# Kernel tuning notes

Hardware: AMD Instinct MI355X
Metric: run time of the kernel (lower is better)

Reference implementation:

```python
import jax, jax.numpy as jnp
import numpy as np

ALPHA = 0.2  # LeakyReLU negative slope


def setup_inputs() -> dict:
    key = jax.random.key(0)
    ks = jax.random.split(key, 6)
    B, N, F_IN, F_OUT = 4, 4096, 128, 128
    return {
        "input": jax.random.normal(ks[0], (B, N, F_IN), dtype=jnp.float32),
        "adj": jax.random.uniform(ks[1], (B, N, N), dtype=jnp.float32),
        "W": jax.random.normal(ks[2], (F_IN, F_OUT), dtype=jnp.float32) * (np.sqrt(2.0) / np.sqrt(F_IN)),
        "a1": jax.random.normal(ks[3], (F_OUT, 1), dtype=jnp.float32) * 0.1,
        "a2": jax.random.normal(ks[4], (F_OUT, 1), dtype=jnp.float32) * 0.1,
        "bias": jax.random.normal(ks[5], (N, F_OUT), dtype=jnp.float32) * 0.02,
    }


def reference(input, adj, W, a1, a2, bias):
    # h = X @ W : [B, N, F_out]
    h = jnp.einsum("bnf,fo->bno", input, W)
    # additive attention scores: e[b,i,j] = leakyrelu(f1[b,i] + f2[b,j])
    f1 = h @ a1            # [B, N, 1]
    f2 = h @ a2            # [B, N, 1]
    e = f1 + jnp.swapaxes(f2, 1, 2)        # [B, N, N]
    e = jnp.where(e >= 0, e, ALPHA * e)    # LeakyReLU
    # NOTE: original multiplies adj into scores (not -inf masking) and
    # softmaxes over dim=1 (the first node axis), faithfully reproduced.
    attention = jax.nn.softmax(adj * e, axis=1)  # [B, N, N]
    # dropout p=0 / eval mode -> identity
    h_prime = jnp.einsum("bij,bjo->bio", attention, h) + bias[None, :, :]
    # in_features == out_features -> plain residual
    return h_prime + input
```

## Files before the change

kernel.cpp:

```cpp
#include <hip/hip_runtime.h>
#include <hip/hip_bf16.h>

typedef short short8 __attribute__((ext_vector_type(8)));
typedef float f32x4 __attribute__((ext_vector_type(4)));
typedef unsigned short u16;
typedef u16 u16x8 __attribute__((ext_vector_type(8)));

static constexpr float kAlpha = 0.2f;

static __device__ inline u16 f2bf(float f) {
  __hip_bfloat16 h = __float2bfloat16(f);
  return *reinterpret_cast<u16*>(&h);
}
static __device__ inline float bf2f(u16 v) {
  unsigned int u = ((unsigned int)v) << 16;
  return __uint_as_float(u);
}

__global__ __launch_bounds__(256) void k1_hW(const float* __restrict__ X,
                                             const float* __restrict__ W,
                                             u16* __restrict__ hbT) {
  int row0 = blockIdx.x * 8;
  int o = threadIdx.x & 127;
  int g = threadIdx.x >> 7;
  __shared__ float Xs[8][128];
#pragma unroll
  for (int s = 0; s < 4; ++s) {
    int idx = threadIdx.x + s * 256;
    Xs[idx >> 7][idx & 127] = X[(size_t)row0 * 128 + idx];
  }
  __syncthreads();
  float acc[4] = {0.f, 0.f, 0.f, 0.f};
  for (int k = 0; k < 128; ++k) {
    float w = W[k * 128 + o];
#pragma unroll
    for (int s = 0; s < 4; ++s) acc[s] += Xs[g + 2 * s][k] * w;
  }
  int b = row0 >> 12;
  int n0 = row0 & 4095;
#pragma unroll
  for (int s = 0; s < 4; ++s)
    hbT[((size_t)b * 128 + o) * 4096 + n0 + g + 2 * s] = f2bf(acc[s]);
}

__global__ __launch_bounds__(256) void k1b_f(const u16* __restrict__ hbT,
                                             const float* __restrict__ a1,
                                             const float* __restrict__ a2,
                                             float* __restrict__ f1,
                                             float* __restrict__ f2) {
  int idx = blockIdx.x * 256 + threadIdx.x;
  int b = idx >> 12;
  int n = idx & 4095;
  const u16* base = hbT + (size_t)b * 128 * 4096 + n;
  float s1 = 0.f, s2 = 0.f;
  for (int o = 0; o < 128; ++o) {
    float h = bf2f(base[(size_t)o * 4096]);
    s1 += h * a1[o];
    s2 += h * a2[o];
  }
  f1[idx] = s1;
  f2[idx] = s2;
}

__global__ __launch_bounds__(256) void k2_dpart(const float* __restrict__ adj,
                                                const float* __restrict__ f1,
                                                const float* __restrict__ f2,
                                                float* __restrict__ dpart) {
  int bid = blockIdx.x;
  int ic = bid & 31;
  int jt = (bid >> 5) & 15;
  int b = bid >> 9;
  int t = threadIdx.x;
  int c = t & 63, r = t >> 6;
  int j = jt * 256 + c * 4;
  const size_t badj = (size_t)b * 4096 * 4096;
  f32x4 f2v = *reinterpret_cast<const f32x4*>(&f2[b * 4096 + j]);
  const float* f1p = f1 + b * 4096;
  int row0 = ic * 128 + r;
  f32x4 sum = (f32x4){0.f, 0.f, 0.f, 0.f};
#pragma unroll 8
  for (int s = 0; s < 32; ++s) {
    int row = row0 + 4 * s;
    f32x4 a = *reinterpret_cast<const f32x4*>(&adj[badj + (size_t)row * 4096 + j]);
    float f1r = f1p[row];
#pragma unroll
    for (int k = 0; k < 4; ++k) {
      float e = f1r + f2v[k];
      e = e >= 0.f ? e : kAlpha * e;
      sum[k] += __expf(a[k] * e);
    }
  }
  __shared__ f32x4 red[256];
  red[t] = sum;
  __syncthreads();
  if (t < 64) {
    f32x4 tt = red[t] + red[t + 64] + red[t + 128] + red[t + 192];
    *reinterpret_cast<f32x4*>(&dpart[(size_t)(b * 32 + ic) * 4096 + j]) = tt;
  }
}

__global__ __launch_bounds__(256) void k2b_scale(const float* __restrict__ dpart,
                                                 const u16* __restrict__ hbT,
                                                 u16* __restrict__ hs) {
  int idx = blockIdx.x * 256 + threadIdx.x;
  int b = idx >> 12, j = idx & 4095;
  float s = 0.f;
#pragma unroll
  for (int ic = 0; ic < 32; ++ic) s += dpart[(size_t)(b * 32 + ic) * 4096 + j];
  float rd = 1.0f / s;
  const u16* src = hbT + (size_t)b * 128 * 4096 + j;
  u16* dst = hs + (size_t)b * 128 * 4096 + j;
#pragma unroll 4
  for (int o = 0; o < 128; ++o) {
    dst[(size_t)o * 4096] = f2bf(bf2f(src[(size_t)o * 4096]) * rd);
  }
}

#define LROW 72
#define BARRIER()                                     \
  {                                                   \
    asm volatile("s_waitcnt lgkmcnt(0)" ::: "memory"); \
    __builtin_amdgcn_s_barrier();                     \
  }
__global__ __launch_bounds__(512) void k3_out(
    const float* __restrict__ adj, const u16* __restrict__ hs,
    const float* __restrict__ f1, const float* __restrict__ f2,
    const float* __restrict__ bias, const float* __restrict__ input,
    float* __restrict__ out) {
  int bid = blockIdx.x;
  int b = bid >> 6;
  int i0 = (bid & 63) * 64;
  int t = threadIdx.x;
  int lane = t & 63;
  int w = t >> 6;

  __shared__ u16 As[2][64 * LROW];
  __shared__ u16 Bs[2][128 * LROW];
  __shared__ float f2s[4096];

  const size_t badj = (size_t)b * 4096 * 4096;
  const u16* hb = hs + (size_t)b * 128 * 4096;

  {
    const f32x4* src = reinterpret_cast<const f32x4*>(f2 + b * 4096);
    f32x4* dst = reinterpret_cast<f32x4*>(f2s);
    dst[t] = src[t];
    dst[t + 512] = src[t + 512];
  }
  __syncthreads();

  int rr = t >> 3;
  int c0 = (t & 7) * 8;
  int bo = t >> 2;
  int bc0 = (t & 3) * 16;

  float f1v = f1[b * 4096 + i0 + rr];

  f32x4 acc[4];
#pragma unroll
  for (int n = 0; n < 4; ++n) acc[n] = (f32x4){0.f, 0.f, 0.f, 0.f};

  int rg = w & 3;
  int ch = w >> 2;

  f32x4 raA0, raA1, raB0, raB1, raC0, raC1, raD0, raD1;
  u16x8 rbA0, rbA1, rbB0, rbB1, rbC0, rbC1, rbD0, rbD1;

#define PREFETCH(S, J0)                                                              \
  {                                                                                  \
    int jj = (J0) & 4095;          \
    const f32x4* ap = reinterpret_cast<const f32x4*>(                                \
        adj + badj + (size_t)(i0 + rr) * 4096 + jj + c0);                            \
    ra##S##0 = ap[0];                                                                \
    ra##S##1 = ap[1];                                                                \
    const u16x8* bp =                                                                \
        reinterpret_cast<const u16x8*>(hb + (size_t)bo * 4096 + jj + bc0);           \
    rb##S##0 = bp[0];                                                                \
    rb##S##1 = bp[1];                                                                \
  }

#define STORE(S, J0, BUF)                                                            \
  {                                                                                  \
    f32x4 e0 = *reinterpret_cast<const f32x4*>(&f2s[(J0) + c0]);                     \
    f32x4 e1 = *reinterpret_cast<const f32x4*>(&f2s[(J0) + c0 + 4]);                 \
    u16x8 pv;                                                                        \
    _Pragma("unroll") for (int k = 0; k < 4; ++k) {                                  \
      float e = f1v + e0[k];                                                         \
      e = e >= 0.f ? e : kAlpha * e;                                                 \
      pv[k] = f2bf(__expf(ra##S##0[k] * e));                                         \
    }                                                                                \
    _Pragma("unroll") for (int k = 0; k < 4; ++k) {                                  \
      float e = f1v + e1[k];                                                         \
      e = e >= 0.f ? e : kAlpha * e;                                                 \
      pv[k + 4] = f2bf(__expf(ra##S##1[k] * e));                                     \
    }                                                                                \
    *reinterpret_cast<u16x8*>(&As[BUF][rr * LROW + c0]) = pv;                        \
    *reinterpret_cast<u16x8*>(&Bs[BUF][bo * LROW + bc0]) = rb##S##0;                 \
    *reinterpret_cast<u16x8*>(&Bs[BUF][bo * LROW + bc0 + 8]) = rb##S##1;             \
  }

#define DOMFMA(BUF)                                                                  \
  {                                                                                  \
    _Pragma("unroll") for (int kk = 0; kk < 64; kk += 32) {                          \
      short8 af = *reinterpret_cast<const short8*>(                                  \
          &As[BUF][(16 * rg + (lane & 15)) * LROW + kk + (lane >> 4) * 8]);          \
      _Pragma("unroll") for (int n = 0; n < 4; ++n) {                                \
        short8 bf = *reinterpret_cast<const short8*>(                                \
            &Bs[BUF][(64 * ch + n * 16 + (lane & 15)) * LROW + kk +                  \
                     (lane >> 4) * 8]);                                              \
        acc[n] = __builtin_amdgcn_mfma_f32_16x16x32_bf16(af, bf, acc[n], 0, 0, 0);   \
      }                                                                              \
    }                                                                                \
  }

  PREFETCH(A, 0);
  PREFETCH(B, 64);
  PREFETCH(C, 128);
  PREFETCH(D, 192);

  for (int j0 = 0; j0 < 4096; j0 += 256) {
    STORE(A, j0, 0);
    BARRIER();
    DOMFMA(0);
    PREFETCH(A, j0 + 256);
    STORE(B, j0 + 64, 1);
    BARRIER();
    DOMFMA(1);
    PREFETCH(B, j0 + 320);
    STORE(C, j0 + 128, 0);
    BARRIER();
    DOMFMA(0);
    PREFETCH(C, j0 + 384);
    STORE(D, j0 + 192, 1);
    BARRIER();
    DOMFMA(1);
    PREFETCH(D, j0 + 448);
  }

  int colbase = ch * 64 + (lane & 15);
  int rowbase = i0 + rg * 16 + (lane >> 4) * 4;
#pragma unroll
  for (int n = 0; n < 4; ++n) {
    int o = colbase + n * 16;
#pragma unroll
    for (int q = 0; q < 4; ++q) {
      int i = rowbase + q;
      size_t oidx = ((size_t)b * 4096 + i) * 128 + o;
      out[oidx] = acc[n][q] + bias[i * 128 + o] + input[oidx];
    }
  }
}

extern "C" void kernel_launch(void* const* d_in, const int* in_sizes, int n_in,
                              void* d_out, int out_size, void* d_ws, size_t ws_size,
                              hipStream_t stream) {
  const float* input = (const float*)d_in[0];
  const float* adj = (const float*)d_in[1];
  const float* W = (const float*)d_in[2];
  const float* a1 = (const float*)d_in[3];
  const float* a2 = (const float*)d_in[4];
  const float* bias = (const float*)d_in[5];
  float* out = (float*)d_out;

  char* ws = (char*)d_ws;
  u16* hbT = (u16*)(ws);
  float* f1 = (float*)(ws + 4194304);
  float* f2 = (float*)(ws + 4259840);
  float* dpart = (float*)(ws + 4325376);
  u16* hs = (u16*)(ws + 6422528);

  k1_hW<<<2048, 256, 0, stream>>>(input, W, hbT);
  k1b_f<<<64, 256, 0, stream>>>(hbT, a1, a2, f1, f2);
  k2_dpart<<<2048, 256, 0, stream>>>(adj, f1, f2, dpart);
  k2b_scale<<<64, 256, 0, stream>>>(dpart, hbT, hs);
  k3_out<<<256, 512, 0, stream>>>(adj, hs, f1, f2, bias, input, out);
}
```

Measured before the change: 141.5 us.

## Materialize bf16 attention weights once per batch instead of re-reading adj in GEMM

The first pass now writes the exponentiated scores as a bf16 matrix while also computing the softmax column sums. The GEMM kernel then reads that bf16 matrix directly as its A operand. This removes the second full fp32 read of adj and the recomputation of exp. The work runs per batch so each 32MB score buffer can stay resident in the large last-level cache between producer and consumer. The GEMM also gains a 4-way split over K, with a separate reduction kernel that adds bias and the residual. In exchange it issues four times as many launches, puts fewer blocks in each one (the scale kernel gets only 16), and writes and re-reads the partial sums.

```diff
diff --git a/kernel.cpp b/kernel.cpp
--- a/kernel.cpp
+++ b/kernel.cpp
@@ -4,6 +4,7 @@
 typedef short short8 __attribute__((ext_vector_type(8)));
 typedef float f32x4 __attribute__((ext_vector_type(4)));
 typedef unsigned short u16;
+typedef u16 u16x4 __attribute__((ext_vector_type(4)));
 typedef u16 u16x8 __attribute__((ext_vector_type(8)));
 
 static constexpr float kAlpha = 0.2f;
@@ -62,100 +63,81 @@
   f2[idx] = s2;
 }
 
-__global__ __launch_bounds__(256) void k2_dpart(const float* __restrict__ adj,
-                                                const float* __restrict__ f1,
-                                                const float* __restrict__ f2,
-                                                float* __restrict__ dpart) {
+__global__ __launch_bounds__(256) void k2p(const float* __restrict__ adjb,
+                                           const float* __restrict__ f1b,
+                                           const float* __restrict__ f2b,
+                                           u16* __restrict__ ptil,
+                                           float* __restrict__ dpart) {
   int bid = blockIdx.x;
   int ic = bid & 31;
-  int jt = (bid >> 5) & 15;
-  int b = bid >> 9;
+  int jt = bid >> 5;
   int t = threadIdx.x;
   int c = t & 63, r = t >> 6;
   int j = jt * 256 + c * 4;
-  const size_t badj = (size_t)b * 4096 * 4096;
-  f32x4 f2v = *reinterpret_cast<const f32x4*>(&f2[b * 4096 + j]);
-  const float* f1p = f1 + b * 4096;
+  f32x4 f2v = *reinterpret_cast<const f32x4*>(&f2b[j]);
   int row0 = ic * 128 + r;
   f32x4 sum = (f32x4){0.f, 0.f, 0.f, 0.f};
-#pragma unroll 8
+#pragma unroll 4
   for (int s = 0; s < 32; ++s) {
     int row = row0 + 4 * s;
-    f32x4 a = *reinterpret_cast<const f32x4*>(&adj[badj + (size_t)row * 4096 + j]);
-    float f1r = f1p[row];
+    f32x4 a = *reinterpret_cast<const f32x4*>(&adjb[(size_t)row * 4096 + j]);
+    float f1r = f1b[row];
+    u16x4 pv;
 #pragma unroll
     for (int k = 0; k < 4; ++k) {
       float e = f1r + f2v[k];
       e = e >= 0.f ? e : kAlpha * e;
-      sum[k] += __expf(a[k] * e);
+      float p = __expf(a[k] * e);
+      sum[k] += p;
+      pv[k] = f2bf(p);
     }
+    *reinterpret_cast<u16x4*>(&ptil[(size_t)row * 4096 + j]) = pv;
   }
   __shared__ f32x4 red[256];
   red[t] = sum;
   __syncthreads();
   if (t < 64) {
     f32x4 tt = red[t] + red[t + 64] + red[t + 128] + red[t + 192];
-    *reinterpret_cast<f32x4*>(&dpart[(size_t)(b * 32 + ic) * 4096 + j]) = tt;
-  }
-}
-
-__global__ __launch_bounds__(256) void k2b_scale(const float* __restrict__ dpart,
-                                                 const u16* __restrict__ hbT,
-                                                 u16* __restrict__ hs) {
-  int idx = blockIdx.x * 256 + threadIdx.x;
-  int b = idx >> 12, j = idx & 4095;
+    *reinterpret_cast<f32x4*>(&dpart[(size_t)ic * 4096 + j]) = tt;
+  }
+}
+
+__global__ __launch_bounds__(256) void k2bs(const float* __restrict__ dpart,
+                                            const u16* __restrict__ hbTb,
+                                            u16* __restrict__ hs) {
+  int j = blockIdx.x * 256 + threadIdx.x;
   float s = 0.f;
 #pragma unroll
-  for (int ic = 0; ic < 32; ++ic) s += dpart[(size_t)(b * 32 + ic) * 4096 + j];
+  for (int ic = 0; ic < 32; ++ic) s += dpart[(size_t)ic * 4096 + j];
   float rd = 1.0f / s;
-  const u16* src = hbT + (size_t)b * 128 * 4096 + j;
-  u16* dst = hs + (size_t)b * 128 * 4096 + j;
 #pragma unroll 4
   for (int o = 0; o < 128; ++o) {
-    dst[(size_t)o * 4096] = f2bf(bf2f(src[(size_t)o * 4096]) * rd);
+    hs[(size_t)o * 4096 + j] = f2bf(bf2f(hbTb[(size_t)o * 4096 + j]) * rd);
   }
 }
 
 #define LROW 72
-#define BARRIER()                                     \
-  {                                                   \
+#define BARRIER()                                      \
+  {                                                    \
     asm volatile("s_waitcnt lgkmcnt(0)" ::: "memory"); \
-    __builtin_amdgcn_s_barrier();                     \
-  }
-__global__ __launch_bounds__(512) void k3_out(
-    const float* __restrict__ adj, const u16* __restrict__ hs,
-    const float* __restrict__ f1, const float* __restrict__ f2,
-    const float* __restrict__ bias, const float* __restrict__ input,
-    float* __restrict__ out) {
+    __builtin_amdgcn_s_barrier();                      \
+  }
+__global__ __launch_bounds__(512) void k3p(const u16* __restrict__ ptil,
+                                           const u16* __restrict__ hs,
+                                           float* __restrict__ parts) {
   int bid = blockIdx.x;
-  int b = bid >> 6;
   int i0 = (bid & 63) * 64;
+  int q = bid >> 6;
+  int jbase = q * 1024;
   int t = threadIdx.x;
   int lane = t & 63;
   int w = t >> 6;
 
-  __shared__ u16 As[2][64 * LROW];
   __shared__ u16 Bs[2][128 * LROW];
-  __shared__ float f2s[4096];
-
-  const size_t badj = (size_t)b * 4096 * 4096;
-  const u16* hb = hs + (size_t)b * 128 * 4096;
-
-  {
-    const f32x4* src = reinterpret_cast<const f32x4*>(f2 + b * 4096);
-    f32x4* dst = reinterpret_cast<f32x4*>(f2s);
-    dst[t] = src[t];
-    dst[t + 512] = src[t + 512];
-  }
-  __syncthreads();
-
-  int rr = t >> 3;
-  int c0 = (t & 7) * 8;
+
   int bo = t >> 2;
   int bc0 = (t & 3) * 16;
 
-  float f1v = f1[b * 4096 + i0 + rr];
-
   f32x4 acc[4];
 #pragma unroll
   for (int n = 0; n < 4; ++n) acc[n] = (f32x4){0.f, 0.f, 0.f, 0.f};
@@ -163,92 +145,94 @@
   int rg = w & 3;
   int ch = w >> 2;
 
-  f32x4 raA0, raA1, raB0, raB1, raC0, raC1, raD0, raD1;
+  const u16* arow = ptil + (size_t)(i0 + 16 * rg + (lane & 15)) * 4096 + (lane >> 4) * 8;
+
+  u16x8 afA0, afA1, afB0, afB1, afC0, afC1, afD0, afD1;
   u16x8 rbA0, rbA1, rbB0, rbB1, rbC0, rbC1, rbD0, rbD1;
 
-#define PREFETCH(S, J0)                                                              \
+#define PREFETCH(S, J0)                                                     \
+  {                                                                         \
+    int jj = (J0) & 4095;          \
+    af##S##0 = *reinterpret_cast<const u16x8*>(arow + jj);                  \
+    af##S##1 = *reinterpret_cast<const u16x8*>(arow + jj + 32);             \
+    const u16x8* bp =                                                       \
+        reinterpret_cast<const u16x8*>(hs + (size_t)bo * 4096 + jj + bc0);  \
+    rb##S##0 = bp[0];                                                       \
+    rb##S##1 = bp[1];                                                       \
+  }
+
+#define STORE(S, BUF)                                                       \
+  {                                                                         \
+    *reinterpret_cast<u16x8*>(&Bs[BUF][bo * LROW + bc0]) = rb##S##0;        \
+    *reinterpret_cast<u16x8*>(&Bs[BUF][bo * LROW + bc0 + 8]) = rb##S##1;    \
+  }
+
+#define DOMFMA(BUF, S)                                                               \
   {                                                                                  \
-    int jj = (J0) & 4095;          \
-    const f32x4* ap = reinterpret_cast<const f32x4*>(                                \
-        adj + badj + (size_t)(i0 + rr) * 4096 + jj + c0);                            \
-    ra##S##0 = ap[0];                                                                \
-    ra##S##1 = ap[1];                                                                \
-    const u16x8* bp =                                                                \
-        reinterpret_cast<const u16x8*>(hb + (size_t)bo * 4096 + jj + bc0);           \
-    rb##S##0 = bp[0];                                                                \
-    rb##S##1 = bp[1];                                                                \
-  }
-
-#define STORE(S, J0, BUF)                                                            \
-  {                                                                                  \
-    f32x4 e0 = *reinterpret_cast<const f32x4*>(&f2s[(J0) + c0]);                     \
-    f32x4 e1 = *reinterpret_cast<const f32x4*>(&f2s[(J0) + c0 + 4]);                 \
-    u16x8 pv;                                                                        \
-    _Pragma("unroll") for (int k = 0; k < 4; ++k) {                                  \
-      float e = f1v + e0[k];                                                         \
-      e = e >= 0.f ? e : kAlpha * e;                                                 \
-      pv[k] = f2bf(__expf(ra##S##0[k] * e));                                         \
+    _Pragma("unroll") for (int n = 0; n < 4; ++n) {                                  \
+      short8 bf = *reinterpret_cast<const short8*>(                                  \
+          &Bs[BUF][(64 * ch + n * 16 + (lane & 15)) * LROW + (lane >> 4) * 8]);      \
+      acc[n] = __builtin_amdgcn_mfma_f32_16x16x32_bf16(                              \
+          *reinterpret_cast<const short8*>(&af##S##0), bf, acc[n], 0, 0, 0);         \
     }                                                                                \
-    _Pragma("unroll") for (int k = 0; k < 4; ++k) {                                  \
-      float e = f1v + e1[k];                                                         \
-      e = e >= 0.f ? e : kAlpha * e;                                                 \
-      pv[k + 4] = f2bf(__expf(ra##S##1[k] * e));                                     \
+    _Pragma("unroll") for (int n = 0; n < 4; ++n) {                                  \
+      short8 bf = *reinterpret_cast<const short8*>(                                  \
+          &Bs[BUF][(64 * ch + n * 16 + (lane & 15)) * LROW + 32 + (lane >> 4) * 8]); \
+      acc[n] = __builtin_amdgcn_mfma_f32_16x16x32_bf16(                              \
+          *reinterpret_cast<const short8*>(&af##S##1), bf, acc[n], 0, 0, 0);         \
     }                                                                                \
-    *reinterpret_cast<u16x8*>(&As[BUF][rr * LROW + c0]) = pv;                        \
-    *reinterpret_cast<u16x8*>(&Bs[BUF][bo * LROW + bc0]) = rb##S##0;                 \
-    *reinterpret_cast<u16x8*>(&Bs[BUF][bo * LROW + bc0 + 8]) = rb##S##1;             \
-  }
-
-#define DOMFMA(BUF)                                                                  \
-  {                                                                                  \
-    _Pragma("unroll") for (int kk = 0; kk < 64; kk += 32) {                          \
-      short8 af = *reinterpret_cast<const short8*>(                                  \
-          &As[BUF][(16 * rg + (lane & 15)) * LROW + kk + (lane >> 4) * 8]);          \
-      _Pragma("unroll") for (int n = 0; n < 4; ++n) {                                \
-        short8 bf = *reinterpret_cast<const short8*>(                                \
-            &Bs[BUF][(64 * ch + n * 16 + (lane & 15)) * LROW + kk +                  \
-                     (lane >> 4) * 8]);                                              \
-        acc[n] = __builtin_amdgcn_mfma_f32_16x16x32_bf16(af, bf, acc[n], 0, 0, 0);   \
-      }                                                                              \
-    }                                                                                \
-  }
-
-  PREFETCH(A, 0);
-  PREFETCH(B, 64);
-  PREFETCH(C, 128);
-  PREFETCH(D, 192);
-
-  for (int j0 = 0; j0 < 4096; j0 += 256) {
-    STORE(A, j0, 0);
-    BARRIER();
-    DOMFMA(0);
+  }
+
+  PREFETCH(A, jbase);
+  PREFETCH(B, jbase + 64);
+  PREFETCH(C, jbase + 128);
+  PREFETCH(D, jbase + 192);
+
+  for (int j0 = jbase; j0 < jbase + 1024; j0 += 256) {
+    STORE(A, 0);
+    BARRIER();
+    DOMFMA(0, A);
     PREFETCH(A, j0 + 256);
-    STORE(B, j0 + 64, 1);
-    BARRIER();
-    DOMFMA(1);
+    STORE(B, 1);
+    BARRIER();
+    DOMFMA(1, B);
     PREFETCH(B, j0 + 320);
-    STORE(C, j0 + 128, 0);
-    BARRIER();
-    DOMFMA(0);
+    STORE(C, 0);
+    BARRIER();
+    DOMFMA(0, C);
     PREFETCH(C, j0 + 384);
-    STORE(D, j0 + 192, 1);
-    BARRIER();
-    DOMFMA(1);
+    STORE(D, 1);
+    BARRIER();
+    DOMFMA(1, D);
     PREFETCH(D, j0 + 448);
   }
 
   int colbase = ch * 64 + (lane & 15);
   int rowbase = i0 + rg * 16 + (lane >> 4) * 4;
+  float* pq = parts + (size_t)q * 4096 * 128;
 #pragma unroll
   for (int n = 0; n < 4; ++n) {
     int o = colbase + n * 16;
 #pragma unroll
-    for (int q = 0; q < 4; ++q) {
-      int i = rowbase + q;
-      size_t oidx = ((size_t)b * 4096 + i) * 128 + o;
-      out[oidx] = acc[n][q] + bias[i * 128 + o] + input[oidx];
+    for (int qq = 0; qq < 4; ++qq) {
+      pq[(size_t)(rowbase + qq) * 128 + o] = acc[n][qq];
     }
   }
+}
+
+__global__ __launch_bounds__(256) void k4r(const float* __restrict__ parts,
+                                           const float* __restrict__ bias,
+                                           const float* __restrict__ inputb,
+                                           float* __restrict__ outb) {
+  size_t v = (size_t)blockIdx.x * 256 + threadIdx.x;
+  size_t e = v * 4;
+  f32x4 s = *reinterpret_cast<const f32x4*>(&parts[e]);
+  s += *reinterpret_cast<const f32x4*>(&parts[e + 524288]);
+  s += *reinterpret_cast<const f32x4*>(&parts[e + 2 * 524288]);
+  s += *reinterpret_cast<const f32x4*>(&parts[e + 3 * 524288]);
+  s += *reinterpret_cast<const f32x4*>(&bias[e]);
+  s += *reinterpret_cast<const f32x4*>(&inputb[e]);
+  *reinterpret_cast<f32x4*>(&outb[e]) = s;
 }
 
 extern "C" void kernel_launch(void* const* d_in, const int* in_sizes, int n_in,
@@ -267,11 +251,24 @@
   float* f1 = (float*)(ws + 4194304);
   float* f2 = (float*)(ws + 4259840);
   float* dpart = (float*)(ws + 4325376);
-  u16* hs = (u16*)(ws + 6422528);
+  u16* hs = (u16*)(ws + 4849664);
+  u16* ptil = (u16*)(ws + 5898240);
+  float* parts = (float*)(ws + 39452672);
 
   k1_hW<<<2048, 256, 0, stream>>>(input, W, hbT);
   k1b_f<<<64, 256, 0, stream>>>(hbT, a1, a2, f1, f2);
-  k2_dpart<<<2048, 256, 0, stream>>>(adj, f1, f2, dpart);
-  k2b_scale<<<64, 256, 0, stream>>>(dpart, hbT, hs);
-  k3_out<<<256, 512, 0, stream>>>(adj, hs, f1, f2, bias, input, out);
-}
+
+  for (int b = 0; b < 4; ++b) {
+    const float* adjb = adj + (size_t)b * 4096 * 4096;
+    const float* f1b = f1 + b * 4096;
+    const float* f2b = f2 + b * 4096;
+    const u16* hbTb = hbT + (size_t)b * 128 * 4096;
+    const float* inputb = input + (size_t)b * 4096 * 128;
+    float* outb = out + (size_t)b * 4096 * 128;
+
+    k2p<<<512, 256, 0, stream>>>(adjb, f1b, f2b, ptil, dpart);
+    k2bs<<<16, 256, 0, stream>>>(dpart, hbTb, hs);
+    k3p<<<256, 512, 0, stream>>>(ptil, hs, parts);
+    k4r<<<512, 256, 0, stream>>>(parts, bias, inputb, outb);
+  }
+}
```

After: 207.9 us. +46.9%, slower.

## Halve k3 row tile to double grid, split k2b across output groups

Applied to the files above, without the earlier changes.

k3_out now handles 32 rows per block instead of 64, which doubles the grid to 512 blocks. Block IDs are remapped to spread batches across XCDs, and the f2 shared-memory staging is dropped in favour of per-tile register loads. Each wave computes a 16x32 output instead of 16x64. k2b_scale is split into 512 blocks, each covering 16 output features, so the small scaling kernel fills more CUs. The smaller tile reloads the hs B-tile for twice as many blocks, so L2 traffic on the h matrix rises.

```diff
diff --git a/kernel.cpp b/kernel.cpp
--- a/kernel.cpp
+++ b/kernel.cpp
@@ -4,6 +4,7 @@
 typedef short short8 __attribute__((ext_vector_type(8)));
 typedef float f32x4 __attribute__((ext_vector_type(4)));
 typedef unsigned short u16;
+typedef u16 u16x4 __attribute__((ext_vector_type(4)));
 typedef u16 u16x8 __attribute__((ext_vector_type(8)));
 
 static constexpr float kAlpha = 0.2f;
@@ -102,8 +103,11 @@
 __global__ __launch_bounds__(256) void k2b_scale(const float* __restrict__ dpart,
                                                  const u16* __restrict__ hbT,
                                                  u16* __restrict__ hs) {
-  int idx = blockIdx.x * 256 + threadIdx.x;
-  int b = idx >> 12, j = idx & 4095;
+  int bid = blockIdx.x;
+  int og = bid & 7;
+  int jb = (bid >> 3) & 15;
+  int b = bid >> 7;
+  int j = jb * 256 + threadIdx.x;
   float s = 0.f;
 #pragma unroll
   for (int ic = 0; ic < 32; ++ic) s += dpart[(size_t)(b * 32 + ic) * 4096 + j];
@@ -111,106 +115,93 @@
   const u16* src = hbT + (size_t)b * 128 * 4096 + j;
   u16* dst = hs + (size_t)b * 128 * 4096 + j;
 #pragma unroll 4
-  for (int o = 0; o < 128; ++o) {
+  for (int o = og * 16; o < og * 16 + 16; ++o) {
     dst[(size_t)o * 4096] = f2bf(bf2f(src[(size_t)o * 4096]) * rd);
   }
 }
 
 #define LROW 72
-#define BARRIER()                                     \
-  {                                                   \
+#define BARRIER()                                      \
+  {                                                    \
     asm volatile("s_waitcnt lgkmcnt(0)" ::: "memory"); \
-    __builtin_amdgcn_s_barrier();                     \
-  }
-__global__ __launch_bounds__(512) void k3_out(
+    __builtin_amdgcn_s_barrier();                      \
+  }
+__global__ __launch_bounds__(512, 4) void k3_out(
     const float* __restrict__ adj, const u16* __restrict__ hs,
     const float* __restrict__ f1, const float* __restrict__ f2,
     const float* __restrict__ bias, const float* __restrict__ input,
     float* __restrict__ out) {
-  int bid = blockIdx.x;
-  int b = bid >> 6;
-  int i0 = (bid & 63) * 64;
+  int bid0 = blockIdx.x;
+  int bid = ((bid0 & 7) << 6) | (bid0 >> 3);
+  int b = bid >> 7;
+  int i0 = (bid & 127) * 32;
   int t = threadIdx.x;
   int lane = t & 63;
   int w = t >> 6;
 
-  __shared__ u16 As[2][64 * LROW];
+  __shared__ u16 As[2][32 * LROW];
   __shared__ u16 Bs[2][128 * LROW];
-  __shared__ float f2s[4096];
 
   const size_t badj = (size_t)b * 4096 * 4096;
   const u16* hb = hs + (size_t)b * 128 * 4096;
-
-  {
-    const f32x4* src = reinterpret_cast<const f32x4*>(f2 + b * 4096);
-    f32x4* dst = reinterpret_cast<f32x4*>(f2s);
-    dst[t] = src[t];
-    dst[t + 512] = src[t + 512];
-  }
-  __syncthreads();
-
-  int rr = t >> 3;
-  int c0 = (t & 7) * 8;
+  const float* f2b = f2 + b * 4096;
+
+  int rr = t >> 4;
+  int c0 = (t & 15) * 4;
   int bo = t >> 2;
   int bc0 = (t & 3) * 16;
 
   float f1v = f1[b * 4096 + i0 + rr];
 
-  f32x4 acc[4];
-#pragma unroll
-  for (int n = 0; n < 4; ++n) acc[n] = (f32x4){0.f, 0.f, 0.f, 0.f};
-
-  int rg = w & 3;
-  int ch = w >> 2;
-
-  f32x4 raA0, raA1, raB0, raB1, raC0, raC1, raD0, raD1;
+  int rg = w & 1;
+  int ch = w >> 1;
+  int l15 = lane & 15;
+  int l8 = (lane >> 4) * 8;
+
+  f32x4 acc[2];
+#pragma unroll
+  for (int n = 0; n < 2; ++n) acc[n] = (f32x4){0.f, 0.f, 0.f, 0.f};
+
+  f32x4 raA, raB, raC, raD;
+  f32x4 rfA, rfB, rfC, rfD;
   u16x8 rbA0, rbA1, rbB0, rbB1, rbC0, rbC1, rbD0, rbD1;
 
-#define PREFETCH(S, J0)                                                              \
-  {                                                                                  \
-    int jj = (J0) & 4095;          \
-    const f32x4* ap = reinterpret_cast<const f32x4*>(                                \
-        adj + badj + (size_t)(i0 + rr) * 4096 + jj + c0);                            \
-    ra##S##0 = ap[0];                                                                \
-    ra##S##1 = ap[1];                                                                \
-    const u16x8* bp =                                                                \
-        reinterpret_cast<const u16x8*>(hb + (size_t)bo * 4096 + jj + bc0);           \
-    rb##S##0 = bp[0];                                                                \
-    rb##S##1 = bp[1];                                                                \
-  }
-
-#define STORE(S, J0, BUF)                                                            \
-  {                                                                                  \
-    f32x4 e0 = *reinterpret_cast<const f32x4*>(&f2s[(J0) + c0]);                     \
-    f32x4 e1 = *reinterpret_cast<const f32x4*>(&f2s[(J0) + c0 + 4]);                 \
-    u16x8 pv;                                                                        \
-    _Pragma("unroll") for (int k = 0; k < 4; ++k) {                                  \
-      float e = f1v + e0[k];                                                         \
-      e = e >= 0.f ? e : kAlpha * e;                                                 \
-      pv[k] = f2bf(__expf(ra##S##0[k] * e));                                         \
-    }                                                                                \
-    _Pragma("unroll") for (int k = 0; k < 4; ++k) {                                  \
-      float e = f1v + e1[k];                                                         \
-      e = e >= 0.f ? e : kAlpha * e;                                                 \
-      pv[k + 4] = f2bf(__expf(ra##S##1[k] * e));                                     \
-    }                                                                                \
-    *reinterpret_cast<u16x8*>(&As[BUF][rr * LROW + c0]) = pv;                        \
-    *reinterpret_cast<u16x8*>(&Bs[BUF][bo * LROW + bc0]) = rb##S##0;                 \
-    *reinterpret_cast<u16x8*>(&Bs[BUF][bo * LROW + bc0 + 8]) = rb##S##1;             \
-  }
-
-#define DOMFMA(BUF)                                                                  \
-  {                                                                                  \
-    _Pragma("unroll") for (int kk = 0; kk < 64; kk += 32) {                          \
-      short8 af = *reinterpret_cast<const short8*>(                                  \
-          &As[BUF][(16 * rg + (lane & 15)) * LROW + kk + (lane >> 4) * 8]);          \
-      _Pragma("unroll") for (int n = 0; n < 4; ++n) {                                \
-        short8 bf = *reinterpret_cast<const short8*>(                                \
-            &Bs[BUF][(64 * ch + n * 16 + (lane & 15)) * LROW + kk +                  \
-                     (lane >> 4) * 8]);                                              \
-        acc[n] = __builtin_amdgcn_mfma_f32_16x16x32_bf16(af, bf, acc[n], 0, 0, 0);   \
-      }                                                                              \
-    }                                                                                \
+#define PREFETCH(S, J0)                                                    \
+  {                                                                        \
+    int jj = (J0) & 4095;         \
+    ra##S = *reinterpret_cast<const f32x4*>(                               \
+        adj + badj + (size_t)(i0 + rr) * 4096 + jj + c0);                  \
+    rf##S = *reinterpret_cast<const f32x4*>(f2b + jj + c0);                \
+    const u16x8* bp =                                                      \
+        reinterpret_cast<const u16x8*>(hb + (size_t)bo * 4096 + jj + bc0); \
+    rb##S##0 = bp[0];                                                      \
+    rb##S##1 = bp[1];                                                      \
+  }
+
+#define STORE(S, BUF)                                                    \
+  {                                                                      \
+    u16x4 pv;                                                            \
+    _Pragma("unroll") for (int k = 0; k < 4; ++k) {                      \
+      float e = f1v + rf##S[k];                                          \
+      e = e >= 0.f ? e : kAlpha * e;                                     \
+      pv[k] = f2bf(__expf(ra##S[k] * e));                                \
+    }                                                                    \
+    *reinterpret_cast<u16x4*>(&As[BUF][rr * LROW + c0]) = pv;            \
+    *reinterpret_cast<u16x8*>(&Bs[BUF][bo * LROW + bc0]) = rb##S##0;     \
+    *reinterpret_cast<u16x8*>(&Bs[BUF][bo * LROW + bc0 + 8]) = rb##S##1; \
+  }
+
+#define DOMFMA(BUF)                                                                \
+  {                                                                                \
+    _Pragma("unroll") for (int kk = 0; kk < 64; kk += 32) {                        \
+      short8 af = *reinterpret_cast<const short8*>(                                \
+          &As[BUF][(16 * rg + l15) * LROW + kk + l8]);                             \
+      _Pragma("unroll") for (int n = 0; n < 2; ++n) {                              \
+        short8 bf = *reinterpret_cast<const short8*>(                              \
+            &Bs[BUF][(32 * ch + n * 16 + l15) * LROW + kk + l8]);                  \
+        acc[n] = __builtin_amdgcn_mfma_f32_16x16x32_bf16(af, bf, acc[n], 0, 0, 0); \
+      }                                                                            \
+    }                                                                              \
   }
 
   PREFETCH(A, 0);
@@ -219,28 +210,28 @@
   PREFETCH(D, 192);
 
   for (int j0 = 0; j0 < 4096; j0 += 256) {
-    STORE(A, j0, 0);
+    STORE(A, 0);
     BARRIER();
     DOMFMA(0);
     PREFETCH(A, j0 + 256);
-    STORE(B, j0 + 64, 1);
+    STORE(B, 1);
     BARRIER();
     DOMFMA(1);
     PREFETCH(B, j0 + 320);
-    STORE(C, j0 + 128, 0);
+    STORE(C, 0);
     BARRIER();
     DOMFMA(0);
     PREFETCH(C, j0 + 384);
-    STORE(D, j0 + 192, 1);
+    STORE(D, 1);
     BARRIER();
     DOMFMA(1);
     PREFETCH(D, j0 + 448);
   }
 
-  int colbase = ch * 64 + (lane & 15);
+  int colbase = 32 * ch + l15;
   int rowbase = i0 + rg * 16 + (lane >> 4) * 4;
 #pragma unroll
-  for (int n = 0; n < 4; ++n) {
+  for (int n = 0; n < 2; ++n) {
     int o = colbase + n * 16;
 #pragma unroll
     for (int q = 0; q < 4; ++q) {
@@ -272,6 +263,6 @@
   k1_hW<<<2048, 256, 0, stream>>>(input, W, hbT);
   k1b_f<<<64, 256, 0, stream>>>(hbT, a1, a2, f1, f2);
   k2_dpart<<<2048, 256, 0, stream>>>(adj, f1, f2, dpart);
-  k2b_scale<<<64, 256, 0, stream>>>(dpart, hbT, hs);
-  k3_out<<<256, 512, 0, stream>>>(adj, hs, f1, f2, bias, input, out);
-}
+  k2b_scale<<<512, 256, 0, stream>>>(dpart, hbT, hs);
+  k3_out<<<512, 512, 0, stream>>>(adj, hs, f1, f2, bias, input, out);
+}
```

New measurement: 144.1 us. No clear change (+1.8%).
